# Performance work log

Measured on AMD Instinct MI355X. Metric: run time of the kernel, lower is better.

## Reference

```python
import jax, jax.numpy as jnp
import numpy as np

B, N, C = 4, 4096, 256
H, D, K = 8, 32, 16  # heads, dim_head, knn


def setup_inputs() -> dict:
    key = jax.random.key(0)
    ks = jax.random.split(key, 7)
    s = 1.0 / np.sqrt(C)
    return {
        "x": jax.random.normal(ks[0], (B, N, C), dtype=jnp.float32),
        "Wq": jax.random.normal(ks[1], (C, H * D), dtype=jnp.float32) * s,
        "bq": jnp.zeros((H * D,), dtype=jnp.float32),
        "Wk": jax.random.normal(ks[2], (C, H * D), dtype=jnp.float32) * s,
        "bk": jnp.zeros((H * D,), dtype=jnp.float32),
        "Wv": jax.random.normal(ks[3], (C, H * D), dtype=jnp.float32) * s,
        "bv": jnp.zeros((H * D,), dtype=jnp.float32),
    }


def _knn_indices(x):
    # squared euclidean distances per batch: [B, N, N]
    sq = jnp.sum(x * x, axis=-1)
    d2 = sq[:, :, None] + sq[:, None, :] - 2.0 * jnp.einsum("bnc,bmc->bnm", x, x)
    # exclude self-loops (loop=False)
    eye = jnp.eye(x.shape[1], dtype=bool)
    d2 = jnp.where(eye[None], jnp.inf, d2)
    # k nearest neighbors (smallest distance)
    _, idx = jax.lax.top_k(-d2, K)  # [B, N, K]
    return idx


def reference(x, Wq, bq, Wk, bk, Wv, bv):
    idx = _knn_indices(x)  # [B, N, K] neighbor (source) node ids per target node
    # gather neighbor features: [B, N, K, C]
    xj = jax.vmap(lambda xb, ib: xb[ib])(x, idx)
    q = (x @ Wq + bq).reshape(B, N, H, D)           # target-node queries
    ke = (xj @ Wk + bk).reshape(B, N, K, H, D)      # per-edge keys
    ve = (xj @ Wv + bv).reshape(B, N, K, H, D)      # per-edge values
    scale = 1.0 / np.sqrt(D)
    scores = jnp.einsum("bnhd,bnkhd->bnkh", q, ke) * scale
    alpha = jax.nn.softmax(scores, axis=2)          # softmax over each node's K neighbors
    out = jnp.einsum("bnkh,bnkhd->bnhd", alpha, ve)
    return out.reshape(B, N, H * D)
```

## Files before the change

kernel.cpp:

```cpp
#include <hip/hip_runtime.h>
#include <cstdint>
#include <cstddef>

#define N_ 4096
#define C_ 256

typedef _Float16 h8 __attribute__((ext_vector_type(8)));
typedef _Float16 h4 __attribute__((ext_vector_type(4)));
typedef float f4 __attribute__((ext_vector_type(4)));

__device__ __forceinline__ void gl2lds16(const void* g, void* l) {
  __builtin_amdgcn_global_load_lds((const __attribute__((address_space(1))) void*)g,
                                   (__attribute__((address_space(3))) void*)l, 16, 0, 0);
}

__device__ __forceinline__ void ce_asc(double& a, double& b) {
  double mn = fmin(a, b), mx = fmax(a, b);
  a = mn; b = mx;
}

__device__ __forceinline__ void sort8_asc(double* c) {
#pragma unroll
  for (int k = 2; k <= 8; k <<= 1)
#pragma unroll
    for (int j = k >> 1; j > 0; j >>= 1)
#pragma unroll
      for (int i = 0; i < 8; i++) {
        int l = i ^ j;
        if (l > i) {
          bool up = ((i & k) == 0);
          double a = c[i], b = c[l];
          double mn = fmin(a, b), mx = fmax(a, b);
          c[i] = up ? mn : mx;
          c[l] = up ? mx : mn;
        }
      }
}

__device__ __forceinline__ void merge8_top16(double* karr, const double* c) {
#pragma unroll
  for (int i = 0; i < 8; i++)
    karr[8 + i] = fmin(karr[8 + i], c[7 - i]);
#pragma unroll
  for (int j = 8; j > 0; j >>= 1)
#pragma unroll
    for (int i = 0; i < 16; i++) {
      int l = i ^ j;
      if (l > i) ce_asc(karr[i], karr[l]);
    }
}

__device__ __forceinline__ void merge16d(double* a, const double* b) {
#pragma unroll
  for (int i = 0; i < 16; i++) a[i] = fmin(a[i], b[15 - i]);
#pragma unroll
  for (int j = 8; j > 0; j >>= 1)
#pragma unroll
    for (int i = 0; i < 16; i++) {
      int l = i ^ j;
      if (l > i) {
        double mn = fmin(a[i], a[l]), mx = fmax(a[i], a[l]);
        a[i] = mn; a[l] = mx;
      }
    }
}

__global__ __launch_bounds__(256) void k_prep(const float* __restrict__ x,
                                              float* __restrict__ sq,
                                              _Float16* __restrict__ xh,
                                              _Float16* __restrict__ xl) {
  int wave = threadIdx.x >> 6, lane = threadIdx.x & 63;
  int row = blockIdx.x * 4 + wave;
  size_t off = (size_t)row * C_ + lane * 4;
  float4 v = *(const float4*)(x + off);
  h4 hi; hi[0] = (_Float16)v.x; hi[1] = (_Float16)v.y;
         hi[2] = (_Float16)v.z; hi[3] = (_Float16)v.w;
  h4 lo; lo[0] = (_Float16)(v.x - (float)hi[0]); lo[1] = (_Float16)(v.y - (float)hi[1]);
         lo[2] = (_Float16)(v.z - (float)hi[2]); lo[3] = (_Float16)(v.w - (float)hi[3]);
  *(h4*)(xh + off) = hi;
  *(h4*)(xl + off) = lo;
  float s = v.x * v.x + v.y * v.y + v.z * v.z + v.w * v.w;
  s += __shfl_xor(s, 32); s += __shfl_xor(s, 16); s += __shfl_xor(s, 8);
  s += __shfl_xor(s, 4);  s += __shfl_xor(s, 2);  s += __shfl_xor(s, 1);
  if (lane == 0) sq[row] = s;
}

__global__ __launch_bounds__(256) void k_wsplit(const float* __restrict__ Wq,
                                                const float* __restrict__ Wk,
                                                const float* __restrict__ Wv,
                                                _Float16* __restrict__ wh,
                                                _Float16* __restrict__ wl) {
  int g = blockIdx.x * 256 + threadIdx.x;
  int m = g >> 16, e = g & 65535;
  int k = e >> 8, j = e & 255;
  const float* W = (m == 0) ? Wq : ((m == 1) ? Wk : Wv);
  float v = W[k * 256 + j];
  _Float16 hi = (_Float16)v;
  _Float16 lo = (_Float16)(v - (float)hi);
  wh[m * 65536 + j * 256 + k] = hi;
  wl[m * 65536 + j * 256 + k] = lo;
}

__global__ __launch_bounds__(256, 2) void k_fused(const _Float16* __restrict__ xh,
                                                  const _Float16* __restrict__ xl,
                                                  const float* __restrict__ sq,
                                                  double* __restrict__ pd,
                                                  const _Float16* __restrict__ wh,
                                                  const _Float16* __restrict__ wl,
                                                  const float* __restrict__ bqp,
                                                  const float* __restrict__ bkp,
                                                  const float* __restrict__ bvp,
                                                  float* __restrict__ qf,
                                                  float* __restrict__ kf,
                                                  float* __restrict__ vf) {
  int gid = blockIdx.x;
  int g5 = gid % 5;
  int tid = threadIdx.x;
  int wave = tid >> 6, lane = tid & 63, quad = lane >> 4, l16 = lane & 15;

  if (g5 < 2) {
    __shared__ __align__(16) _Float16 Bh[16 * 528];
    __shared__ __align__(16) _Float16 Bl[16 * 528];
    __shared__ __align__(16) float sc[128 * 36];
    __shared__ float sqS[32];

    int bid = (gid / 5) * 2 + g5;
    int s4 = bid & 3, tile = (bid >> 2) & 31, b = bid >> 7;
    int bN = b * N_, n0 = tile * 128, src0g = s4 * 1024;

    h8 Ah[2][8], Al[2][8];
    int tb = bN + n0 + wave * 32;
#pragma unroll
    for (int rt = 0; rt < 2; rt++)
#pragma unroll
      for (int kc = 0; kc < 8; kc++) {
        size_t off = (size_t)(tb + rt * 16 + l16) * C_ + kc * 32 + quad * 8;
        Ah[rt][kc] = *(const h8*)(xh + off);
        Al[rt][kc] = *(const h8*)(xl + off);
      }
    float sqT[2][4];
#pragma unroll
    for (int rt = 0; rt < 2; rt++)
#pragma unroll
      for (int i = 0; i < 4; i++)
        sqT[rt][i] = sq[tb + rt * 16 + quad * 4 + i];

    double karr[16];
#pragma unroll
    for (int p = 0; p < 16; p++) karr[p] = 1e300;
    int rowo = tid & 127, half = tid >> 7;

    {
      const _Float16* gh = xh + (size_t)(bN + src0g) * C_ + lane * 8;
      const _Float16* gl = xl + (size_t)(bN + src0g) * C_ + lane * 8;
#pragma unroll
      for (int k = 0; k < 4; k++) {
        int seg = wave * 4 + k;
        gl2lds16(gh + seg * 512, &Bh[seg * 528]);
        gl2lds16(gl + seg * 512, &Bl[seg * 528]);
      }
      if (tid < 32) sqS[tid] = sq[bN + src0g + tid];
    }

    int hb0 = ((l16 >> 1) * 528) + ((l16 & 1) * 256) + quad * 8;
    int hb1 = (((16 + l16) >> 1) * 528) + ((l16 & 1) * 256) + quad * 8;

#pragma unroll 1
    for (int ch = 0; ch < 32; ch++) {
      int src0 = src0g + ch * 32;
      __syncthreads();

      f4 acc[2][2];
#pragma unroll
      for (int rt = 0; rt < 2; rt++)
#pragma unroll
        for (int ct = 0; ct < 2; ct++) acc[rt][ct] = f4{0.f, 0.f, 0.f, 0.f};
#pragma unroll
      for (int kc = 0; kc < 8; kc++) {
        h8 bh0 = *(const h8*)(&Bh[hb0 + kc * 32]);
        h8 bh1 = *(const h8*)(&Bh[hb1 + kc * 32]);
        h8 bl0 = *(const h8*)(&Bl[hb0 + kc * 32]);
        h8 bl1 = *(const h8*)(&Bl[hb1 + kc * 32]);
#pragma unroll
        for (int rt = 0; rt < 2; rt++) {
          acc[rt][0] = __builtin_amdgcn_mfma_f32_16x16x32_f16(Ah[rt][kc], bh0, acc[rt][0], 0, 0, 0);
          acc[rt][0] = __builtin_amdgcn_mfma_f32_16x16x32_f16(Ah[rt][kc], bl0, acc[rt][0], 0, 0, 0);
          acc[rt][0] = __builtin_amdgcn_mfma_f32_16x16x32_f16(Al[rt][kc], bh0, acc[rt][0], 0, 0, 0);
          acc[rt][1] = __builtin_amdgcn_mfma_f32_16x16x32_f16(Ah[rt][kc], bh1, acc[rt][1], 0, 0, 0);
          acc[rt][1] = __builtin_amdgcn_mfma_f32_16x16x32_f16(Ah[rt][kc], bl1, acc[rt][1], 0, 0, 0);
          acc[rt][1] = __builtin_amdgcn_mfma_f32_16x16x32_f16(Al[rt][kc], bh1, acc[rt][1], 0, 0, 0);
        }
      }
      float sqSr[2] = {sqS[l16], sqS[16 + l16]};
#pragma unroll
      for (int rt = 0; rt < 2; rt++)
#pragma unroll
        for (int ct = 0; ct < 2; ct++) {
          int c = ct * 16 + l16;
#pragma unroll
          for (int i = 0; i < 4; i++) {
            int r = wave * 32 + rt * 16 + quad * 4 + i;
            float d2 = sqT[rt][i] + sqSr[ct] - 2.0f * acc[rt][ct][i];
            if (n0 + r == src0 + c) d2 = 1e38f;
            sc[r * 36 + c] = d2;
          }
        }
      __syncthreads();

      if (ch < 31) {
        int srcn = src0 + 32;
        const _Float16* gh = xh + (size_t)(bN + srcn) * C_ + lane * 8;
        const _Float16* gl = xl + (size_t)(bN + srcn) * C_ + lane * 8;
#pragma unroll
        for (int k = 0; k < 4; k++) {
          int seg = wave * 4 + k;
          gl2lds16(gh + seg * 512, &Bh[seg * 528]);
          gl2lds16(gl + seg * 512, &Bl[seg * 528]);
        }
        if (tid < 32) sqS[tid] = sq[bN + srcn + tid];
      }

#pragma unroll
      for (int bt = 0; bt < 2; bt++) {
        float dv[8];
#pragma unroll
        for (int k4 = 0; k4 < 2; k4++)
          *(float4*)&dv[k4 * 4] = *(const float4*)(&sc[rowo * 36 + half * 16 + bt * 8 + k4 * 4]);
        double c8[8];
#pragma unroll
        for (int j = 0; j < 8; j++) {
          double key = (double)dv[j];
          c8[j] = __longlong_as_double(__double_as_longlong(key) |
                                       (unsigned)(src0 + half * 16 + bt * 8 + j));
        }
        sort8_asc(c8);
        merge8_top16(karr, c8);
      }
    }

    __syncthreads();
    double* scd = (double*)sc;
    if (tid >= 128) {
#pragma unroll
      for (int p = 0; p < 16; p++) scd[(tid - 128) * 17 + p] = karr[p];
    }
    __syncthreads();
    if (tid < 128) {
#pragma unroll
      for (int i = 0; i < 16; i++)
        karr[i] = fmin(karr[i], scd[tid * 17 + (15 - i)]);
#pragma unroll
      for (int j = 8; j > 0; j >>= 1)
#pragma unroll
        for (int i = 0; i < 16; i++) {
          int l = i ^ j;
          if (l > i) ce_asc(karr[i], karr[l]);
        }
#pragma unroll
      for (int p = 0; p < 16; p++)
        pd[((size_t)bid * 128 + tid) * 16 + p] = karr[p];
    }
  } else {
    int pbid = (gid / 5) * 3 + (g5 - 2);
    int m   = pbid >> 8;
    int rb  = (pbid >> 1) & 127;
    int cp  = pbid & 1;
    const float* bb = (m == 0) ? bqp : ((m == 1) ? bkp : bvp);
    float* dst      = (m == 0) ? qf  : ((m == 1) ? kf  : vf);
    int row0 = rb * 128 + wave * 32;

    h8 Ah[2][8], Al[2][8];
#pragma unroll
    for (int rt = 0; rt < 2; rt++)
#pragma unroll
      for (int kc = 0; kc < 8; kc++) {
        size_t off = (size_t)(row0 + rt * 16 + l16) * C_ + kc * 32 + quad * 8;
        Ah[rt][kc] = *(const h8*)(xh + off);
        Al[rt][kc] = *(const h8*)(xl + off);
      }
    const _Float16* whm = wh + (size_t)m * 65536;
    const _Float16* wlm = wl + (size_t)m * 65536;

    f4 acc[2][8];
#pragma unroll
    for (int rt = 0; rt < 2; rt++)
#pragma unroll
      for (int ct = 0; ct < 8; ct++) acc[rt][ct] = f4{0.f, 0.f, 0.f, 0.f};
#pragma unroll
    for (int kc = 0; kc < 8; kc++) {
#pragma unroll
      for (int ct = 0; ct < 8; ct++) {
        int col = cp * 128 + ct * 16 + l16;
        h8 bh = *(const h8*)(whm + (size_t)col * 256 + kc * 32 + quad * 8);
        h8 bl = *(const h8*)(wlm + (size_t)col * 256 + kc * 32 + quad * 8);
#pragma unroll
        for (int rt = 0; rt < 2; rt++) {
          acc[rt][ct] = __builtin_amdgcn_mfma_f32_16x16x32_f16(Ah[rt][kc], bh, acc[rt][ct], 0, 0, 0);
          acc[rt][ct] = __builtin_amdgcn_mfma_f32_16x16x32_f16(Ah[rt][kc], bl, acc[rt][ct], 0, 0, 0);
          acc[rt][ct] = __builtin_amdgcn_mfma_f32_16x16x32_f16(Al[rt][kc], bh, acc[rt][ct], 0, 0, 0);
        }
      }
    }
#pragma unroll
    for (int rt = 0; rt < 2; rt++)
#pragma unroll
      for (int ct = 0; ct < 8; ct++) {
        int col = cp * 128 + ct * 16 + l16;
        float bias = bb[col];
#pragma unroll
        for (int i = 0; i < 4; i++) {
          int r = row0 + rt * 16 + quad * 4 + i;
          dst[(size_t)r * C_ + col] = acc[rt][ct][i] + bias;
        }
      }
  }
}

__global__ __launch_bounds__(64) void k_kmerge(const double* __restrict__ pd,
                                               int* __restrict__ idxo) {
  int g = blockIdx.x * 64 + threadIdx.x;
  int b = g >> 12, n = g & 4095;
  int tile = n >> 7, r = n & 127;
  size_t base = (size_t)(((b * 32 + tile) * 4) * 128 + r) * 16;

  double acc[16], other[16];
#pragma unroll
  for (int p = 0; p < 16; p++) acc[p] = pd[base + p];
#pragma unroll
  for (int s = 1; s < 4; s++) {
    size_t bs = base + (size_t)s * 128 * 16;
#pragma unroll
    for (int p = 0; p < 16; p++) other[p] = pd[bs + p];
    merge16d(acc, other);
  }
#pragma unroll
  for (int k = 0; k < 16; k++)
    idxo[(size_t)g * 16 + k] = (int)(__double_as_longlong(acc[k]) & 0xFFF);
}

__global__ __launch_bounds__(256) void k_attn(const float* __restrict__ qf,
                                              const float* __restrict__ kf,
                                              const float* __restrict__ vf,
                                              const int* __restrict__ idxv,
                                              float* __restrict__ out) {
  int wave = threadIdx.x >> 6, lane = threadIdx.x & 63;
  int g = blockIdx.x * 4 + wave;
  int bN = (g >> 12) << 12;
  float4 q4 = *(const float4*)(qf + (size_t)g * C_ + lane * 4);
  int my = idxv[(size_t)g * 16 + (lane & 15)];
  const float scale = 0.17677669529663687f;

  float s[16];
  float4 vv[16];
#pragma unroll
  for (int j = 0; j < 16; j++) {
    int nb = __shfl(my, j);
    size_t base = (size_t)(bN + nb) * C_ + lane * 4;
    float4 k4 = *(const float4*)(kf + base);
    vv[j] = *(const float4*)(vf + base);
    float p = k4.x * q4.x + k4.y * q4.y + k4.z * q4.z + k4.w * q4.w;
    p += __shfl_xor(p, 1); p += __shfl_xor(p, 2); p += __shfl_xor(p, 4);
    s[j] = p * scale;
  }
  float mx = s[0];
#pragma unroll
  for (int j = 1; j < 16; j++) mx = fmaxf(mx, s[j]);
  float den = 0.f;
#pragma unroll
  for (int j = 0; j < 16; j++) { s[j] = __expf(s[j] - mx); den += s[j]; }
  float inv = 1.0f / den;
  float4 o; o.x = 0.f; o.y = 0.f; o.z = 0.f; o.w = 0.f;
#pragma unroll
  for (int j = 0; j < 16; j++) {
    float w = s[j] * inv;
    o.x = fmaf(w, vv[j].x, o.x); o.y = fmaf(w, vv[j].y, o.y);
    o.z = fmaf(w, vv[j].z, o.z); o.w = fmaf(w, vv[j].w, o.w);
  }
  *(float4*)(out + (size_t)g * C_ + lane * 4) = o;
}

extern "C" void kernel_launch(void* const* d_in, const int* in_sizes, int n_in,
                              void* d_out, int out_size, void* d_ws, size_t ws_size,
                              hipStream_t stream) {
  const float* x  = (const float*)d_in[0];
  const float* Wq = (const float*)d_in[1];
  const float* bq = (const float*)d_in[2];
  const float* Wk = (const float*)d_in[3];
  const float* bk = (const float*)d_in[4];
  const float* Wv = (const float*)d_in[5];
  const float* bv = (const float*)d_in[6];
  float* out = (float*)d_out;

  char* ws = (char*)d_ws;
  float*     sqp  = (float*)(ws + 0);
  _Float16*  xh   = (_Float16*)(ws + 65536);
  _Float16*  xl   = (_Float16*)(ws + 8454144);
  float*     qf   = (float*)(ws + 16842752);
  float*     kf   = (float*)(ws + 33619968);
  float*     vf   = (float*)(ws + 50397184);
  double*    pd   = (double*)(ws + 67174400);
  int*       idxb = (int*)  (ws + 75563008);
  _Float16*  whf  = (_Float16*)(ws + 76611584);
  _Float16*  wlf  = (_Float16*)(ws + 77004800);

  k_prep  <<<4096, 256, 0, stream>>>(x, sqp, xh, xl);
  k_wsplit<<<768,  256, 0, stream>>>(Wq, Wk, Wv, whf, wlf);
  k_fused <<<1280, 256, 0, stream>>>(xh, xl, sqp, pd, whf, wlf,
                                     bq, bk, bv, qf, kf, vf);
  k_kmerge<<<256,  64,  0, stream>>>(pd, idxb);
  k_attn  <<<4096, 256, 0, stream>>>(qf, kf, vf, idxb, out);
}
```

Before: 323.3 us.

## Split fused kNN/projection kernel and store K/V projections in fp16

The heterogeneous fused kernel, which interleaved kNN-distance blocks with QKV projection blocks, is split into two separate launches: k_proj (occupancy hint 3) and k_knn. The K and V projections are now written as fp16 instead of fp32, which halves both the write traffic and the random gather traffic in the attention kernel. The risk is fp16 rounding error in keys and values, and the loss of any overlap the fused kernel got from running the two kinds of work side by side.

```diff
diff --git a/kernel.cpp b/kernel.cpp
--- a/kernel.cpp
+++ b/kernel.cpp
@@ -101,218 +101,220 @@
   wl[m * 65536 + j * 256 + k] = lo;
 }
 
-__global__ __launch_bounds__(256, 2) void k_fused(const _Float16* __restrict__ xh,
-                                                  const _Float16* __restrict__ xl,
-                                                  const float* __restrict__ sq,
-                                                  double* __restrict__ pd,
-                                                  const _Float16* __restrict__ wh,
-                                                  const _Float16* __restrict__ wl,
-                                                  const float* __restrict__ bqp,
-                                                  const float* __restrict__ bkp,
-                                                  const float* __restrict__ bvp,
-                                                  float* __restrict__ qf,
-                                                  float* __restrict__ kf,
-                                                  float* __restrict__ vf) {
-  int gid = blockIdx.x;
-  int g5 = gid % 5;
+__global__ __launch_bounds__(256, 3) void k_proj(const _Float16* __restrict__ xh,
+                                                 const _Float16* __restrict__ xl,
+                                                 const _Float16* __restrict__ wh,
+                                                 const _Float16* __restrict__ wl,
+                                                 const float* __restrict__ bqp,
+                                                 const float* __restrict__ bkp,
+                                                 const float* __restrict__ bvp,
+                                                 float* __restrict__ qf,
+                                                 _Float16* __restrict__ kh,
+                                                 _Float16* __restrict__ vh) {
+  int tid = threadIdx.x;
+  int bid = blockIdx.x;
+  int m   = bid >> 8;
+  int rb  = (bid >> 1) & 127;
+  int cp  = bid & 1;
+  int wave = tid >> 6, lane = tid & 63, quad = lane >> 4, l16 = lane & 15;
+  const float* bb = (m == 0) ? bqp : ((m == 1) ? bkp : bvp);
+  int row0 = rb * 128 + wave * 32;
+
+  h8 Ah[2][8], Al[2][8];
+#pragma unroll
+  for (int rt = 0; rt < 2; rt++)
+#pragma unroll
+    for (int kc = 0; kc < 8; kc++) {
+      size_t off = (size_t)(row0 + rt * 16 + l16) * C_ + kc * 32 + quad * 8;
+      Ah[rt][kc] = *(const h8*)(xh + off);
+      Al[rt][kc] = *(const h8*)(xl + off);
+    }
+  const _Float16* whm = wh + (size_t)m * 65536;
+  const _Float16* wlm = wl + (size_t)m * 65536;
+
+  f4 acc[2][8];
+#pragma unroll
+  for (int rt = 0; rt < 2; rt++)
+#pragma unroll
+    for (int ct = 0; ct < 8; ct++) acc[rt][ct] = f4{0.f, 0.f, 0.f, 0.f};
+#pragma unroll
+  for (int kc = 0; kc < 8; kc++) {
+#pragma unroll
+    for (int ct = 0; ct < 8; ct++) {
+      int col = cp * 128 + ct * 16 + l16;
+      h8 bh = *(const h8*)(whm + (size_t)col * 256 + kc * 32 + quad * 8);
+      h8 bl = *(const h8*)(wlm + (size_t)col * 256 + kc * 32 + quad * 8);
+#pragma unroll
+      for (int rt = 0; rt < 2; rt++) {
+        acc[rt][ct] = __builtin_amdgcn_mfma_f32_16x16x32_f16(Ah[rt][kc], bh, acc[rt][ct], 0, 0, 0);
+        acc[rt][ct] = __builtin_amdgcn_mfma_f32_16x16x32_f16(Ah[rt][kc], bl, acc[rt][ct], 0, 0, 0);
+        acc[rt][ct] = __builtin_amdgcn_mfma_f32_16x16x32_f16(Al[rt][kc], bh, acc[rt][ct], 0, 0, 0);
+      }
+    }
+  }
+  _Float16* d16 = (m == 1) ? kh : vh;
+#pragma unroll
+  for (int rt = 0; rt < 2; rt++)
+#pragma unroll
+    for (int ct = 0; ct < 8; ct++) {
+      int col = cp * 128 + ct * 16 + l16;
+      float bias = bb[col];
+#pragma unroll
+      for (int i = 0; i < 4; i++) {
+        int r = row0 + rt * 16 + quad * 4 + i;
+        float o = acc[rt][ct][i] + bias;
+        if (m == 0) qf[(size_t)r * C_ + col] = o;
+        else        d16[(size_t)r * C_ + col] = (_Float16)o;
+      }
+    }
+}
+
+__global__ __launch_bounds__(256, 2) void k_knn(const _Float16* __restrict__ xh,
+                                                const _Float16* __restrict__ xl,
+                                                const float* __restrict__ sq,
+                                                double* __restrict__ pd) {
+  __shared__ __align__(16) _Float16 Bh[16 * 528];
+  __shared__ __align__(16) _Float16 Bl[16 * 528];
+  __shared__ __align__(16) float sc[128 * 36];
+  __shared__ float sqS[32];
+
   int tid = threadIdx.x;
   int wave = tid >> 6, lane = tid & 63, quad = lane >> 4, l16 = lane & 15;
-
-  if (g5 < 2) {
-    __shared__ __align__(16) _Float16 Bh[16 * 528];
-    __shared__ __align__(16) _Float16 Bl[16 * 528];
-    __shared__ __align__(16) float sc[128 * 36];
-    __shared__ float sqS[32];
-
-    int bid = (gid / 5) * 2 + g5;
-    int s4 = bid & 3, tile = (bid >> 2) & 31, b = bid >> 7;
-    int bN = b * N_, n0 = tile * 128, src0g = s4 * 1024;
-
-    h8 Ah[2][8], Al[2][8];
-    int tb = bN + n0 + wave * 32;
+  int bid = blockIdx.x;
+  int s4 = bid & 3, tile = (bid >> 2) & 31, b = bid >> 7;
+  int bN = b * N_, n0 = tile * 128, src0g = s4 * 1024;
+
+  h8 Ah[2][8], Al[2][8];
+  int tb = bN + n0 + wave * 32;
+#pragma unroll
+  for (int rt = 0; rt < 2; rt++)
+#pragma unroll
+    for (int kc = 0; kc < 8; kc++) {
+      size_t off = (size_t)(tb + rt * 16 + l16) * C_ + kc * 32 + quad * 8;
+      Ah[rt][kc] = *(const h8*)(xh + off);
+      Al[rt][kc] = *(const h8*)(xl + off);
+    }
+  float sqT[2][4];
+#pragma unroll
+  for (int rt = 0; rt < 2; rt++)
+#pragma unroll
+    for (int i = 0; i < 4; i++)
+      sqT[rt][i] = sq[tb + rt * 16 + quad * 4 + i];
+
+  double karr[16];
+#pragma unroll
+  for (int p = 0; p < 16; p++) karr[p] = 1e300;
+  int rowo = tid & 127, half = tid >> 7;
+
+  {
+    const _Float16* gh = xh + (size_t)(bN + src0g) * C_ + lane * 8;
+    const _Float16* gl = xl + (size_t)(bN + src0g) * C_ + lane * 8;
+#pragma unroll
+    for (int k = 0; k < 4; k++) {
+      int seg = wave * 4 + k;
+      gl2lds16(gh + seg * 512, &Bh[seg * 528]);
+      gl2lds16(gl + seg * 512, &Bl[seg * 528]);
+    }
+    if (tid < 32) sqS[tid] = sq[bN + src0g + tid];
+  }
+
+  int hb0 = ((l16 >> 1) * 528) + ((l16 & 1) * 256) + quad * 8;
+  int hb1 = (((16 + l16) >> 1) * 528) + ((l16 & 1) * 256) + quad * 8;
+
+#pragma unroll 1
+  for (int ch = 0; ch < 32; ch++) {
+    int src0 = src0g + ch * 32;
+    __syncthreads();
+
+    f4 acc[2][2];
 #pragma unroll
     for (int rt = 0; rt < 2; rt++)
 #pragma unroll
-      for (int kc = 0; kc < 8; kc++) {
-        size_t off = (size_t)(tb + rt * 16 + l16) * C_ + kc * 32 + quad * 8;
-        Ah[rt][kc] = *(const h8*)(xh + off);
-        Al[rt][kc] = *(const h8*)(xl + off);
-      }
-    float sqT[2][4];
+      for (int ct = 0; ct < 2; ct++) acc[rt][ct] = f4{0.f, 0.f, 0.f, 0.f};
+#pragma unroll
+    for (int kc = 0; kc < 8; kc++) {
+      h8 bh0 = *(const h8*)(&Bh[hb0 + kc * 32]);
+      h8 bh1 = *(const h8*)(&Bh[hb1 + kc * 32]);
+      h8 bl0 = *(const h8*)(&Bl[hb0 + kc * 32]);
+      h8 bl1 = *(const h8*)(&Bl[hb1 + kc * 32]);
+#pragma unroll
+      for (int rt = 0; rt < 2; rt++) {
+        acc[rt][0] = __builtin_amdgcn_mfma_f32_16x16x32_f16(Ah[rt][kc], bh0, acc[rt][0], 0, 0, 0);
+        acc[rt][0] = __builtin_amdgcn_mfma_f32_16x16x32_f16(Ah[rt][kc], bl0, acc[rt][0], 0, 0, 0);
+        acc[rt][0] = __builtin_amdgcn_mfma_f32_16x16x32_f16(Al[rt][kc], bh0, acc[rt][0], 0, 0, 0);
+        acc[rt][1] = __builtin_amdgcn_mfma_f32_16x16x32_f16(Ah[rt][kc], bh1, acc[rt][1], 0, 0, 0);
+        acc[rt][1] = __builtin_amdgcn_mfma_f32_16x16x32_f16(Ah[rt][kc], bl1, acc[rt][1], 0, 0, 0);
+        acc[rt][1] = __builtin_amdgcn_mfma_f32_16x16x32_f16(Al[rt][kc], bh1, acc[rt][1], 0, 0, 0);
+      }
+    }
+    float sqSr[2] = {sqS[l16], sqS[16 + l16]};
 #pragma unroll
     for (int rt = 0; rt < 2; rt++)
 #pragma unroll
-      for (int i = 0; i < 4; i++)
-        sqT[rt][i] = sq[tb + rt * 16 + quad * 4 + i];
-
-    double karr[16];
-#pragma unroll
-    for (int p = 0; p < 16; p++) karr[p] = 1e300;
-    int rowo = tid & 127, half = tid >> 7;
-
-    {
-      const _Float16* gh = xh + (size_t)(bN + src0g) * C_ + lane * 8;
-      const _Float16* gl = xl + (size_t)(bN + src0g) * C_ + lane * 8;
+      for (int ct = 0; ct < 2; ct++) {
+        int c = ct * 16 + l16;
+#pragma unroll
+        for (int i = 0; i < 4; i++) {
+          int r = wave * 32 + rt * 16 + quad * 4 + i;
+          float d2 = sqT[rt][i] + sqSr[ct] - 2.0f * acc[rt][ct][i];
+          if (n0 + r == src0 + c) d2 = 1e38f;
+          sc[r * 36 + c] = d2;
+        }
+      }
+    __syncthreads();
+
+    if (ch < 31) {
+      int srcn = src0 + 32;
+      const _Float16* gh = xh + (size_t)(bN + srcn) * C_ + lane * 8;
+      const _Float16* gl = xl + (size_t)(bN + srcn) * C_ + lane * 8;
 #pragma unroll
       for (int k = 0; k < 4; k++) {
         int seg = wave * 4 + k;
         gl2lds16(gh + seg * 512, &Bh[seg * 528]);
         gl2lds16(gl + seg * 512, &Bl[seg * 528]);
       }
-      if (tid < 32) sqS[tid] = sq[bN + src0g + tid];
-    }
-
-    int hb0 = ((l16 >> 1) * 528) + ((l16 & 1) * 256) + quad * 8;
-    int hb1 = (((16 + l16) >> 1) * 528) + ((l16 & 1) * 256) + quad * 8;
-
-#pragma unroll 1
-    for (int ch = 0; ch < 32; ch++) {
-      int src0 = src0g + ch * 32;
-      __syncthreads();
-
-      f4 acc[2][2];
-#pragma unroll
-      for (int rt = 0; rt < 2; rt++)
-#pragma unroll
-        for (int ct = 0; ct < 2; ct++) acc[rt][ct] = f4{0.f, 0.f, 0.f, 0.f};
-#pragma unroll
-      for (int kc = 0; kc < 8; kc++) {
-        h8 bh0 = *(const h8*)(&Bh[hb0 + kc * 32]);
-        h8 bh1 = *(const h8*)(&Bh[hb1 + kc * 32]);
-        h8 bl0 = *(const h8*)(&Bl[hb0 + kc * 32]);
-        h8 bl1 = *(const h8*)(&Bl[hb1 + kc * 32]);
-#pragma unroll
-        for (int rt = 0; rt < 2; rt++) {
-          acc[rt][0] = __builtin_amdgcn_mfma_f32_16x16x32_f16(Ah[rt][kc], bh0, acc[rt][0], 0, 0, 0);
-          acc[rt][0] = __builtin_amdgcn_mfma_f32_16x16x32_f16(Ah[rt][kc], bl0, acc[rt][0], 0, 0, 0);
-          acc[rt][0] = __builtin_amdgcn_mfma_f32_16x16x32_f16(Al[rt][kc], bh0, acc[rt][0], 0, 0, 0);
-          acc[rt][1] = __builtin_amdgcn_mfma_f32_16x16x32_f16(Ah[rt][kc], bh1, acc[rt][1], 0, 0, 0);
-          acc[rt][1] = __builtin_amdgcn_mfma_f32_16x16x32_f16(Ah[rt][kc], bl1, acc[rt][1], 0, 0, 0);
-          acc[rt][1] = __builtin_amdgcn_mfma_f32_16x16x32_f16(Al[rt][kc], bh1, acc[rt][1], 0, 0, 0);
-        }
-      }
-      float sqSr[2] = {sqS[l16], sqS[16 + l16]};
-#pragma unroll
-      for (int rt = 0; rt < 2; rt++)
-#pragma unroll
-        for (int ct = 0; ct < 2; ct++) {
-          int c = ct * 16 + l16;
-#pragma unroll
-          for (int i = 0; i < 4; i++) {
-            int r = wave * 32 + rt * 16 + quad * 4 + i;
-            float d2 = sqT[rt][i] + sqSr[ct] - 2.0f * acc[rt][ct][i];
-            if (n0 + r == src0 + c) d2 = 1e38f;
-            sc[r * 36 + c] = d2;
-          }
-        }
-      __syncthreads();
-
-      if (ch < 31) {
-        int srcn = src0 + 32;
-        const _Float16* gh = xh + (size_t)(bN + srcn) * C_ + lane * 8;
-        const _Float16* gl = xl + (size_t)(bN + srcn) * C_ + lane * 8;
-#pragma unroll
-        for (int k = 0; k < 4; k++) {
-          int seg = wave * 4 + k;
-          gl2lds16(gh + seg * 512, &Bh[seg * 528]);
-          gl2lds16(gl + seg * 512, &Bl[seg * 528]);
-        }
-        if (tid < 32) sqS[tid] = sq[bN + srcn + tid];
-      }
-
-#pragma unroll
-      for (int bt = 0; bt < 2; bt++) {
-        float dv[8];
-#pragma unroll
-        for (int k4 = 0; k4 < 2; k4++)
-          *(float4*)&dv[k4 * 4] = *(const float4*)(&sc[rowo * 36 + half * 16 + bt * 8 + k4 * 4]);
-        double c8[8];
-#pragma unroll
-        for (int j = 0; j < 8; j++) {
-          double key = (double)dv[j];
-          c8[j] = __longlong_as_double(__double_as_longlong(key) |
-                                       (unsigned)(src0 + half * 16 + bt * 8 + j));
-        }
-        sort8_asc(c8);
-        merge8_top16(karr, c8);
-      }
-    }
-
-    __syncthreads();
-    double* scd = (double*)sc;
-    if (tid >= 128) {
-#pragma unroll
-      for (int p = 0; p < 16; p++) scd[(tid - 128) * 17 + p] = karr[p];
-    }
-    __syncthreads();
-    if (tid < 128) {
-#pragma unroll
-      for (int i = 0; i < 16; i++)
-        karr[i] = fmin(karr[i], scd[tid * 17 + (15 - i)]);
-#pragma unroll
-      for (int j = 8; j > 0; j >>= 1)
-#pragma unroll
-        for (int i = 0; i < 16; i++) {
-          int l = i ^ j;
-          if (l > i) ce_asc(karr[i], karr[l]);
-        }
-#pragma unroll
-      for (int p = 0; p < 16; p++)
-        pd[((size_t)bid * 128 + tid) * 16 + p] = karr[p];
-    }
-  } else {
-    int pbid = (gid / 5) * 3 + (g5 - 2);
-    int m   = pbid >> 8;
-    int rb  = (pbid >> 1) & 127;
-    int cp  = pbid & 1;
-    const float* bb = (m == 0) ? bqp : ((m == 1) ? bkp : bvp);
-    float* dst      = (m == 0) ? qf  : ((m == 1) ? kf  : vf);
-    int row0 = rb * 128 + wave * 32;
-
-    h8 Ah[2][8], Al[2][8];
-#pragma unroll
-    for (int rt = 0; rt < 2; rt++)
-#pragma unroll
-      for (int kc = 0; kc < 8; kc++) {
-        size_t off = (size_t)(row0 + rt * 16 + l16) * C_ + kc * 32 + quad * 8;
-        Ah[rt][kc] = *(const h8*)(xh + off);
-        Al[rt][kc] = *(const h8*)(xl + off);
-      }
-    const _Float16* whm = wh + (size_t)m * 65536;
-    const _Float16* wlm = wl + (size_t)m * 65536;
-
-    f4 acc[2][8];
-#pragma unroll
-    for (int rt = 0; rt < 2; rt++)
-#pragma unroll
-      for (int ct = 0; ct < 8; ct++) acc[rt][ct] = f4{0.f, 0.f, 0.f, 0.f};
-#pragma unroll
-    for (int kc = 0; kc < 8; kc++) {
-#pragma unroll
-      for (int ct = 0; ct < 8; ct++) {
-        int col = cp * 128 + ct * 16 + l16;
-        h8 bh = *(const h8*)(whm + (size_t)col * 256 + kc * 32 + quad * 8);
-        h8 bl = *(const h8*)(wlm + (size_t)col * 256 + kc * 32 + quad * 8);
-#pragma unroll
-        for (int rt = 0; rt < 2; rt++) {
-          acc[rt][ct] = __builtin_amdgcn_mfma_f32_16x16x32_f16(Ah[rt][kc], bh, acc[rt][ct], 0, 0, 0);
-          acc[rt][ct] = __builtin_amdgcn_mfma_f32_16x16x32_f16(Ah[rt][kc], bl, acc[rt][ct], 0, 0, 0);
-          acc[rt][ct] = __builtin_amdgcn_mfma_f32_16x16x32_f16(Al[rt][kc], bh, acc[rt][ct], 0, 0, 0);
-        }
-      }
-    }
-#pragma unroll
-    for (int rt = 0; rt < 2; rt++)
-#pragma unroll
-      for (int ct = 0; ct < 8; ct++) {
-        int col = cp * 128 + ct * 16 + l16;
-        float bias = bb[col];
-#pragma unroll
-        for (int i = 0; i < 4; i++) {
-          int r = row0 + rt * 16 + quad * 4 + i;
-          dst[(size_t)r * C_ + col] = acc[rt][ct][i] + bias;
-        }
-      }
+      if (tid < 32) sqS[tid] = sq[bN + srcn + tid];
+    }
+
+#pragma unroll
+    for (int bt = 0; bt < 2; bt++) {
+      float dv[8];
+#pragma unroll
+      for (int k4 = 0; k4 < 2; k4++)
+        *(float4*)&dv[k4 * 4] = *(const float4*)(&sc[rowo * 36 + half * 16 + bt * 8 + k4 * 4]);
+      double c8[8];
+#pragma unroll
+      for (int j = 0; j < 8; j++) {
+        double key = (double)dv[j];
+        c8[j] = __longlong_as_double(__double_as_longlong(key) |
+                                     (unsigned)(src0 + half * 16 + bt * 8 + j));
+      }
+      sort8_asc(c8);
+      merge8_top16(karr, c8);
+    }
+  }
+
+  __syncthreads();
+  double* scd = (double*)sc;
+  if (tid >= 128) {
+#pragma unroll
+    for (int p = 0; p < 16; p++) scd[(tid - 128) * 17 + p] = karr[p];
+  }
+  __syncthreads();
+  if (tid < 128) {
+#pragma unroll
+    for (int i = 0; i < 16; i++)
+      karr[i] = fmin(karr[i], scd[tid * 17 + (15 - i)]);
+#pragma unroll
+    for (int j = 8; j > 0; j >>= 1)
+#pragma unroll
+      for (int i = 0; i < 16; i++) {
+        int l = i ^ j;
+        if (l > i) ce_asc(karr[i], karr[l]);
+      }
+#pragma unroll
+    for (int p = 0; p < 16; p++)
+      pd[((size_t)bid * 128 + tid) * 16 + p] = karr[p];
   }
 }
 
@@ -339,8 +341,8 @@
 }
 
 __global__ __launch_bounds__(256) void k_attn(const float* __restrict__ qf,
-                                              const float* __restrict__ kf,
-                                              const float* __restrict__ vf,
+                                              const _Float16* __restrict__ kh,
+                                              const _Float16* __restrict__ vh,
                                               const int* __restrict__ idxv,
                                               float* __restrict__ out) {
   int wave = threadIdx.x >> 6, lane = threadIdx.x & 63;
@@ -351,14 +353,15 @@
   const float scale = 0.17677669529663687f;
 
   float s[16];
-  float4 vv[16];
+  h4 vv[16];
 #pragma unroll
   for (int j = 0; j < 16; j++) {
     int nb = __shfl(my, j);
     size_t base = (size_t)(bN + nb) * C_ + lane * 4;
-    float4 k4 = *(const float4*)(kf + base);
-    vv[j] = *(const float4*)(vf + base);
-    float p = k4.x * q4.x + k4.y * q4.y + k4.z * q4.z + k4.w * q4.w;
+    h4 k4 = *(const h4*)(kh + base);
+    vv[j] = *(const h4*)(vh + base);
+    float p = (float)k4[0] * q4.x + (float)k4[1] * q4.y +
+              (float)k4[2] * q4.z + (float)k4[3] * q4.w;
     p += __shfl_xor(p, 1); p += __shfl_xor(p, 2); p += __shfl_xor(p, 4);
     s[j] = p * scale;
   }
@@ -373,8 +376,8 @@
 #pragma unroll
   for (int j = 0; j < 16; j++) {
     float w = s[j] * inv;
-    o.x = fmaf(w, vv[j].x, o.x); o.y = fmaf(w, vv[j].y, o.y);
-    o.z = fmaf(w, vv[j].z, o.z); o.w = fmaf(w, vv[j].w, o.w);
+    o.x = fmaf(w, (float)vv[j][0], o.x); o.y = fmaf(w, (float)vv[j][1], o.y);
+    o.z = fmaf(w, (float)vv[j][2], o.z); o.w = fmaf(w, (float)vv[j][3], o.w);
   }
   *(float4*)(out + (size_t)g * C_ + lane * 4) = o;
 }
@@ -396,8 +399,8 @@
   _Float16*  xh   = (_Float16*)(ws + 65536);
   _Float16*  xl   = (_Float16*)(ws + 8454144);
   float*     qf   = (float*)(ws + 16842752);
-  float*     kf   = (float*)(ws + 33619968);
-  float*     vf   = (float*)(ws + 50397184);
+  _Float16*  khp  = (_Float16*)(ws + 33619968);
+  _Float16*  vhp  = (_Float16*)(ws + 50397184);
   double*    pd   = (double*)(ws + 67174400);
   int*       idxb = (int*)  (ws + 75563008);
   _Float16*  whf  = (_Float16*)(ws + 76611584);
@@ -405,8 +408,8 @@
 
   k_prep  <<<4096, 256, 0, stream>>>(x, sqp, xh, xl);
   k_wsplit<<<768,  256, 0, stream>>>(Wq, Wk, Wv, whf, wlf);
-  k_fused <<<1280, 256, 0, stream>>>(xh, xl, sqp, pd, whf, wlf,
-                                     bq, bk, bv, qf, kf, vf);
+  k_proj  <<<768,  256, 0, stream>>>(xh, xl, whf, wlf, bq, bk, bv, qf, khp, vhp);
+  k_knn   <<<512,  256, 0, stream>>>(xh, xl, sqp, pd);
   k_kmerge<<<256,  64,  0, stream>>>(pd, idxb);
-  k_attn  <<<4096, 256, 0, stream>>>(qf, kf, vf, idxb, out);
-}
+  k_attn  <<<4096, 256, 0, stream>>>(qf, khp, vhp, idxb, out);
+}
```

Result: faster. 284.7 us (-11.9%).
